# Optimization experiments

Measured on AMD Instinct MI355X. Metric: run time of the kernel, lower is better.

## Reference

```python
import jax, jax.numpy as jnp
import numpy as np

H, I = 16, 64
SCALE = 1.0 / (I ** 0.5)

def _rel_shift(x):
    # x: (S, J, B, H) -> Transformer-XL relative shift trick
    S, J, B, Hh = x.shape
    pad = jnp.zeros((S, 1, B, Hh), dtype=x.dtype)
    y = jnp.concatenate([pad, x], axis=1)           # (S, J+1, B, H)
    y = y.reshape(J + 1, S, B, Hh)[1:]              # (J, S, B, H)
    return y.reshape(S, J, B, Hh)

def setup_inputs() -> dict:
    key = jax.random.key(0)
    ks = jax.random.split(key, 10)
    S, P, B, E = 1024, 1024, 4, 1024
    J = P + S
    # causal mask: query s may attend keys j <= P + s; True = blocked
    mask = (jnp.arange(J)[None, :] > (P + jnp.arange(S))[:, None])[..., None]  # (S,J,1) bool
    sc = E ** -0.5
    return {
        "inputMHA": jax.random.normal(ks[0], (S, B, E), jnp.float32),
        "posEmbeddings": jax.random.normal(ks[1], (J, E), jnp.float32),
        "memory": jax.random.normal(ks[2], (P, B, E), jnp.float32),
        "u": jax.random.normal(ks[3], (H, I), jnp.float32) * 0.02,
        "v": jax.random.normal(ks[4], (H, I), jnp.float32) * 0.02,
        "mask": mask,
        "W_kv": jax.random.normal(ks[5], (E, 2 * H * I), jnp.float32) * sc,
        "W_q": jax.random.normal(ks[6], (E, H * I), jnp.float32) * sc,
        "W_p": jax.random.normal(ks[7], (E, H * I), jnp.float32) * sc,
        "W_o": jax.random.normal(ks[8], (H * I, E), jnp.float32) * sc,
        "gamma": jnp.ones((E,), jnp.float32),
        "beta": jnp.zeros((E,), jnp.float32),
    }

def reference(inputMHA, posEmbeddings, memory, u, v, mask, W_kv, W_q, W_p, W_o, gamma, beta):
    S, B, E = inputMHA.shape
    P = memory.shape[0]
    J = P + S
    x = jnp.concatenate([memory, inputMHA], axis=0)          # (J,B,E)
    kv = x @ W_kv                                            # (J,B,2HI)
    keys, values = jnp.split(kv, 2, axis=-1)
    q = (inputMHA @ W_q).reshape(S, B, H, I)                 # (S,B,H,I)
    K = keys.reshape(J, B, H, I)
    content = jnp.einsum('sbhi,jbhi->sjbh', q + u, K)        # content score
    p = (posEmbeddings @ W_p).reshape(J, H, I)               # (J,H,I)
    pos = jnp.einsum('sbhi,jhi->sjbh', q + v, p)             # position score
    pos = _rel_shift(pos)
    attn = content + pos                                     # (S,J,B,H)
    attn = jnp.where(mask[..., None], -jnp.inf, attn)        # mask (S,J,1)->(S,J,1,1)
    attn = jax.nn.softmax(attn * jnp.asarray(SCALE, attn.dtype), axis=1)
    V = values.reshape(J, B, H, I)
    awv = jnp.einsum('sjbh,jbhi->sbhi', attn, V).reshape(S, B, H * I)
    out = inputMHA + awv @ W_o                               # residual (dropout = eval identity)
    mean = jnp.mean(out, axis=-1, keepdims=True)
    var = jnp.var(out, axis=-1, keepdims=True)
    return (out - mean) / jnp.sqrt(var + 1e-5) * gamma + beta
```

## Files before the change

### kernel.cpp

```cpp
#include <hip/hip_runtime.h>
#include <hip/hip_bf16.h>

#define S_ 1024
#define P_ 1024
#define B_ 4
#define E_ 1024
#define J_ 2048
#define H_ 16
#define I_ 64

typedef __bf16 bf16_t;
typedef __bf16 bf16x8 __attribute__((ext_vector_type(8)));
typedef __bf16 bf16x4 __attribute__((ext_vector_type(4)));
typedef unsigned short u16x8 __attribute__((ext_vector_type(8)));
typedef float f32x4 __attribute__((ext_vector_type(4)));

#define MFMA16(a, b, c) __builtin_amdgcn_mfma_f32_16x16x32_bf16(a, b, c, 0, 0, 0)

#define SWZ(r, c) (((r) << 6) + ((((((c) >> 3)) ^ ((r) & 7)) << 3)) + ((c) & 7))

__device__ __forceinline__ void g2l16(const bf16_t* g, bf16_t* l) {
    __builtin_amdgcn_global_load_lds(
        (const __attribute__((address_space(1))) unsigned int*)(const void*)g,
        (__attribute__((address_space(3))) unsigned int*)(void*)l,
        16, 0, 0);
}

__global__ __launch_bounds__(256) void cvt_all_kernel(const float* __restrict__ memory,
                                                      const float* __restrict__ input,
                                                      const float* __restrict__ posEmb,
                                                      bf16_t* __restrict__ Xbf,
                                                      bf16_t* __restrict__ Pemb) {
    int blk = blockIdx.x;
    const float* src;
    bf16_t* dst;
    if (blk < 4096) { src = memory; dst = Xbf; }
    else if (blk < 8192) { blk -= 4096; src = input; dst = Xbf + (size_t)P_ * B_ * E_; }
    else { blk -= 8192; src = posEmb; dst = Pemb; }
    int i = (blk * 256 + threadIdx.x) * 4;
    float4 v = *(const float4*)(src + i);
    bf16x4 o = {(bf16_t)v.x, (bf16_t)v.y, (bf16_t)v.z, (bf16_t)v.w};
    *(bf16x4*)(dst + i) = o;
}

__global__ void trans_all_kernel(const float* __restrict__ W_kv, bf16_t* __restrict__ Wkvt,
                                 const float* __restrict__ W_q, bf16_t* __restrict__ Wqt,
                                 const float* __restrict__ W_p, bf16_t* __restrict__ Wpt,
                                 const float* __restrict__ W_o, bf16_t* __restrict__ Wot) {
    __shared__ float tile[32][33];
    int z = blockIdx.z;
    const float* W = (z == 0) ? W_kv : (z == 1) ? W_q : (z == 2) ? W_p : W_o;
    bf16_t* Wt = (z == 0) ? Wkvt : (z == 1) ? Wqt : (z == 2) ? Wpt : Wot;
    int N = (z == 0) ? 2048 : 1024;
    if (blockIdx.x * 32 >= N) return;
    int n0 = blockIdx.x * 32, k0 = blockIdx.y * 32;
    int x = threadIdx.x, y = threadIdx.y;
    for (int i = 0; i < 32; i += 8)
        tile[y + i][x] = W[(size_t)(k0 + y + i) * N + n0 + x];
    __syncthreads();
    for (int i = 0; i < 32; i += 8)
        Wt[(size_t)(n0 + y + i) * 1024 + k0 + x] = (bf16_t)tile[x][y + i];
}

__device__ __forceinline__ void gemm_tile(
    const bf16_t* __restrict__ A, const bf16_t* __restrict__ Bt, int N,
    int m0, int n0, int epi,
    bf16_t* __restrict__ out0, bf16_t* __restrict__ out1,
    const float* __restrict__ add0, const float* __restrict__ add1,
    float* __restrict__ outf,
    bf16_t* AlL, bf16_t* BlL) {
    const int K = 1024;
    int tid = threadIdx.x;
    int wave = tid >> 6, lane = tid & 63, quad = lane >> 4, l16 = lane & 15;
    int wm = (wave & 1) * 64, wn = (wave >> 1) * 64;
    int lrow = lane >> 3;
    int gsw = ((lane & 7) ^ lrow) << 3;
    f32x4 zero = {0.f, 0.f, 0.f, 0.f};
    f32x4 acc[4][4];
    #pragma unroll
    for (int i = 0; i < 4; i++)
        #pragma unroll
        for (int j = 0; j < 4; j++) acc[i][j] = zero;

    for (int k0 = 0; k0 < K; k0 += 64) {
        __syncthreads();
        #pragma unroll
        for (int r = 0; r < 4; r++) {
            int row0 = r * 32 + wave * 8;
            g2l16(&A[(size_t)(m0 + row0 + lrow) * K + k0 + gsw], &AlL[row0 * 64]);
            g2l16(&Bt[(size_t)(n0 + row0 + lrow) * K + k0 + gsw], &BlL[row0 * 64]);
        }
        __syncthreads();
        #pragma unroll
        for (int ks = 0; ks < 2; ks++) {
            bf16x8 af[4], bfr[4];
            #pragma unroll
            for (int i = 0; i < 4; i++)
                af[i] = *(const bf16x8*)&AlL[SWZ(wm + i * 16 + l16, ks * 32 + quad * 8)];
            #pragma unroll
            for (int j = 0; j < 4; j++)
                bfr[j] = *(const bf16x8*)&BlL[SWZ(wn + j * 16 + l16, ks * 32 + quad * 8)];
            #pragma unroll
            for (int i = 0; i < 4; i++)
                #pragma unroll
                for (int j = 0; j < 4; j++) acc[i][j] = MFMA16(af[i], bfr[j], acc[i][j]);
        }
    }
    #pragma unroll
    for (int i = 0; i < 4; i++)
        #pragma unroll
        for (int j = 0; j < 4; j++)
            #pragma unroll
            for (int reg = 0; reg < 4; reg++) {
                int m = m0 + wm + i * 16 + quad * 4 + reg;
                int n = n0 + wn + j * 16 + l16;
                float v = acc[i][j][reg];
                if (epi == 0) {
                    out0[(size_t)m * N + n] = (bf16_t)v;
                } else if (epi == 1) {
                    out0[(size_t)m * N + n] = (bf16_t)(v + add0[n]);
                    out1[(size_t)m * N + n] = (bf16_t)(v + add1[n]);
                } else {
                    outf[(size_t)m * N + n] = v + add0[(size_t)m * N + n];
                }
            }
}

__global__ __launch_bounds__(256) void gemm3_kernel(
    const bf16_t* __restrict__ Xbf, const bf16_t* __restrict__ Wkvt, bf16_t* __restrict__ kvb,
    const bf16_t* __restrict__ Wqt, bf16_t* __restrict__ qub, bf16_t* __restrict__ qvb,
    const float* __restrict__ u, const float* __restrict__ v,
    const bf16_t* __restrict__ Pemb, const bf16_t* __restrict__ Wpt, bf16_t* __restrict__ pb) {
    __shared__ __attribute__((aligned(16))) bf16_t Al[128 * 64];
    __shared__ __attribute__((aligned(16))) bf16_t Bl[128 * 64];
    int id = blockIdx.x;
    if (id < 1024) {
        gemm_tile(Xbf, Wkvt, 2048, (id >> 4) * 128, (id & 15) * 128, 0,
                  kvb, nullptr, nullptr, nullptr, nullptr, Al, Bl);
    } else if (id < 1280) {
        int t = id - 1024;
        gemm_tile(Xbf + (size_t)P_ * B_ * E_, Wqt, 1024, (t >> 3) * 128, (t & 7) * 128, 1,
                  qub, qvb, u, v, nullptr, Al, Bl);
    } else {
        int t = id - 1280;
        gemm_tile(Pemb, Wpt, 1024, (t >> 3) * 128, (t & 7) * 128, 0,
                  pb, nullptr, nullptr, nullptr, nullptr, Al, Bl);
    }
}

__global__ __launch_bounds__(256) void gemmo_kernel(
    const bf16_t* __restrict__ awvb, const bf16_t* __restrict__ Wot,
    const float* __restrict__ inputMHA, float* __restrict__ opre) {
    __shared__ __attribute__((aligned(16))) bf16_t Al[128 * 64];
    __shared__ __attribute__((aligned(16))) bf16_t Bl[128 * 64];
    int id = blockIdx.x;
    gemm_tile(awvb, Wot, 1024, (id >> 3) * 128, (id & 7) * 128, 2,
              nullptr, nullptr, inputMHA, nullptr, opre, Al, Bl);
}

__global__ __launch_bounds__(256) void flash_kernel(
    const bf16_t* __restrict__ qu, const bf16_t* __restrict__ qv,
    const bf16_t* __restrict__ kv, const bf16_t* __restrict__ pm,
    float* __restrict__ Oacc, float* __restrict__ lacc) {
    __shared__ __attribute__((aligned(16))) bf16_t Klds[64 * 64];
    __shared__ __attribute__((aligned(16))) bf16_t Vt[64 * 64];
    __shared__ __attribute__((aligned(16))) bf16_t Plds[128 * 64];
    __shared__ __attribute__((aligned(16))) bf16_t Prob[4 * 16 * 64];

    int tid = threadIdx.x;
    int wave = tid >> 6, lane = tid & 63, quad = lane >> 4, l16 = lane & 15;

    int x = blockIdx.x;
    int s_blk, c;
    if (x < 24) { s_blk = x / 3; c = x - s_blk * 3; }
    else        { int y = x - 24; s_blk = 8 + (y >> 2); c = y & 3; }
    int nt = 17 + s_blk;
    int t0 = c * 8;
    int t1 = t0 + 8; if (t1 > nt) t1 = nt;

    int s0 = s_blk * 64;
    int bh = blockIdx.y;
    int b = bh >> 4, h = bh & 15;
    int srow0 = s0 + wave * 16;

    const bf16_t* qub = qu + ((size_t)(srow0 + l16) * B_ + b) * 1024 + h * 64 + quad * 8;
    const bf16_t* qvb = qv + ((size_t)(srow0 + l16) * B_ + b) * 1024 + h * 64 + quad * 8;
    bf16x8 aqu0 = *(const bf16x8*)(qub);
    bf16x8 aqu1 = *(const bf16x8*)(qub + 32);
    bf16x8 aqv0 = *(const bf16x8*)(qvb);
    bf16x8 aqv1 = *(const bf16x8*)(qvb + 32);

    f32x4 zero = {0.f, 0.f, 0.f, 0.f};
    f32x4 accO[4];
    #pragma unroll
    for (int ot = 0; ot < 4; ot++) accO[ot] = zero;
    float lrowp[4] = {0.f, 0.f, 0.f, 0.f};

    const int w0u = 960 - s0;
    const int woff = 48 - wave * 16;
    const float SCL = 0.125f * 1.44269504088896f;

    int jr = tid >> 3, seg8g = tid & 7;
    int jp = tid & 31, iseg = tid >> 5;
    uint* VtU = (uint*)&Vt[0];
    bf16_t* ProbW = Prob + (wave << 10);

    {
        int j0 = t0 * 64;
        const bf16_t* kp = kv + ((size_t)(j0 + jr) * B_ + b) * 2048 + h * 64 + seg8g * 8;
        uint4 ka = *(const uint4*)kp;
        uint4 kb = *(const uint4*)(kp + (size_t)32 * B_ * 2048);
        const bf16_t* vp = kv + ((size_t)(j0 + jp * 2) * B_ + b) * 2048 + 1024 + h * 64 + iseg * 8;
        u16x8 va = *(const u16x8*)vp;
        u16x8 vb = *(const u16x8*)(vp + (size_t)B_ * 2048);
        uint4 pd[4];
        #pragma unroll
        for (int r = 0; r < 4; r++) {
            int idx = tid + 256 * r;
            int pr = idx >> 3, pg = idx & 7;
            int lr = w0u + j0 + pr; if (lr > J_ - 1) lr = J_ - 1;
            pd[r] = *(const uint4*)(pm + (size_t)lr * 1024 + h * 64 + pg * 8);
        }
        *(uint4*)&Klds[SWZ(jr, seg8g * 8)] = ka;
        *(uint4*)&Klds[SWZ(jr + 32, seg8g * 8)] = kb;
        #pragma unroll
        for (int e = 0; e < 8; e++) {
            int row = iseg * 8 + e;
            VtU[(row << 5) + ((((jp >> 2) ^ (row & 7)) << 2)) + (jp & 3)] =
                (uint)va[e] | ((uint)vb[e] << 16);
        }
        #pragma unroll
        for (int r = 0; r < 4; r++) {
            int idx = tid + 256 * r;
            int pr = idx >> 3, pg = idx & 7;
            *(uint4*)&Plds[SWZ((w0u + j0 + pr) & 127, pg * 8)] = pd[r];
        }
    }
    __syncthreads();

    for (int it = t0; it < t1; it++) {
        int j0 = it * 64;
        bool pf = (it + 1 < t1);
        uint4 ka, kb, pd0, pd1;
        u16x8 va, vb;
        int pr0 = tid >> 3, pg0 = tid & 7;
        int pr1 = (tid + 256) >> 3, pg1 = tid & 7;
        if (pf) {
            int j1 = j0 + 64;
            const bf16_t* kp = kv + ((size_t)(j1 + jr) * B_ + b) * 2048 + h * 64 + seg8g * 8;
            ka = *(const uint4*)kp;
            kb = *(const uint4*)(kp + (size_t)32 * B_ * 2048);
            const bf16_t* vp = kv + ((size_t)(j1 + jp * 2) * B_ + b) * 2048 + 1024 + h * 64 + iseg * 8;
            va = *(const u16x8*)vp;
            vb = *(const u16x8*)(vp + (size_t)B_ * 2048);
            int lr0 = w0u + j0 + 128 + pr0; if (lr0 > J_ - 1) lr0 = J_ - 1;
            int lr1 = w0u + j0 + 128 + pr1; if (lr1 > J_ - 1) lr1 = J_ - 1;
            pd0 = *(const uint4*)(pm + (size_t)lr0 * 1024 + h * 64 + pg0 * 8);
            pd1 = *(const uint4*)(pm + (size_t)lr1 * 1024 + h * 64 + pg1 * 8);
        }

        f32x4 cs[4];
        #pragma unroll
        for (int t = 0; t < 4; t++) cs[t] = zero;
        __builtin_amdgcn_s_setprio(1);
        #pragma unroll
        for (int ks = 0; ks < 2; ks++) {
            bf16x8 aq = ks ? aqu1 : aqu0;
            #pragma unroll
            for (int t = 0; t < 4; t++) {
                bf16x8 bk = *(const bf16x8*)&Klds[SWZ(t * 16 + l16, ks * 32 + quad * 8)];
                cs[t] = MFMA16(aq, bk, cs[t]);
            }
        }
        f32x4 ep[5];
        #pragma unroll
        for (int t = 0; t < 5; t++) ep[t] = zero;
        #pragma unroll
        for (int ks = 0; ks < 2; ks++) {
            bf16x8 aq = ks ? aqv1 : aqv0;
            #pragma unroll
            for (int t = 0; t < 5; t++) {
                int prow = (w0u + j0 + woff + t * 16 + l16) & 127;
                bf16x8 bp = *(const bf16x8*)&Plds[SWZ(prow, ks * 32 + quad * 8)];
                ep[t] = MFMA16(aq, bp, ep[t]);
            }
        }
        __builtin_amdgcn_s_setprio(0);

        #pragma unroll
        for (int reg = 0; reg < 4; reg++) {
            int r = quad * 4 + reg;
            int s = srow0 + r;
            int idx = l16 + 15 - r;
            int srcl = quad * 16 + (idx & 15);
            float sh[5];
            #pragma unroll
            for (int t = 0; t < 5; t++) sh[t] = __shfl(ep[t][reg], srcl);
            float psum = 0.f;
            #pragma unroll
            for (int t = 0; t < 4; t++) {
                float pos = (idx < 16) ? sh[t] : sh[t + 1];
                float p = exp2f((cs[t][reg] + pos) * SCL);
                p = (j0 + t * 16 + l16 > P_ + s) ? 0.f : p;
                ProbW[SWZ(r, t * 16 + l16)] = (bf16_t)p;
                psum += p;
            }
            lrowp[reg] += psum;
        }

        __builtin_amdgcn_s_setprio(1);
        #pragma unroll
        for (int ks = 0; ks < 2; ks++) {
            bf16x8 pa = *(const bf16x8*)&Prob[(wave << 10) + SWZ(l16, ks * 32 + quad * 8)];
            #pragma unroll
            for (int ot = 0; ot < 4; ot++) {
                bf16x8 bv = *(const bf16x8*)&Vt[SWZ(ot * 16 + l16, ks * 32 + quad * 8)];
                accO[ot] = MFMA16(pa, bv, accO[ot]);
            }
        }
        __builtin_amdgcn_s_setprio(0);

        __syncthreads();
        if (pf) {
            *(uint4*)&Klds[SWZ(jr, seg8g * 8)] = ka;
            *(uint4*)&Klds[SWZ(jr + 32, seg8g * 8)] = kb;
            #pragma unroll
            for (int e2 = 0; e2 < 8; e2++) {
                int row = iseg * 8 + e2;
                VtU[(row << 5) + ((((jp >> 2) ^ (row & 7)) << 2)) + (jp & 3)] =
                    (uint)va[e2] | ((uint)vb[e2] << 16);
            }
            *(uint4*)&Plds[SWZ((w0u + j0 + pr0) & 127, pg0 * 8)] = pd0;
            *(uint4*)&Plds[SWZ((w0u + j0 + pr1) & 127, pg1 * 8)] = pd1;
        }
        __syncthreads();
    }

    #pragma unroll
    for (int reg = 0; reg < 4; reg++) {
        int r = quad * 4 + reg;
        int srow = srow0 + r;
        float l = lrowp[reg];
        #pragma unroll
        for (int d = 1; d < 16; d <<= 1) l += __shfl_xor(l, d);
        if (l16 == 0) atomicAdd(&lacc[((size_t)srow * B_ + b) * H_ + h], l);
        size_t rowoff = ((size_t)srow * B_ + b) * 1024 + h * 64;
        #pragma unroll
        for (int ot = 0; ot < 4; ot++)
            atomicAdd(&Oacc[rowoff + ot * 16 + l16], accO[ot][reg]);
    }
}

__global__ __launch_bounds__(256) void norm_kernel(const float* __restrict__ Oacc,
                                                   const float* __restrict__ lacc,
                                                   bf16_t* __restrict__ awv) {
    int i4 = (blockIdx.x * 256 + threadIdx.x) * 4;
    int row = i4 >> 6;
    float inv = 1.0f / lacc[row];
    float4 o = *(const float4*)(Oacc + i4);
    bf16x4 r = {(bf16_t)(o.x * inv), (bf16_t)(o.y * inv),
                (bf16_t)(o.z * inv), (bf16_t)(o.w * inv)};
    *(bf16x4*)(awv + i4) = r;
}

__global__ __launch_bounds__(256) void ln_kernel(const float* __restrict__ x,
                                                 const float* __restrict__ gamma,
                                                 const float* __restrict__ beta,
                                                 float* __restrict__ out) {
    int row = blockIdx.x, tid = threadIdx.x;
    int lane = tid & 63, wave = tid >> 6;
    float4 v = ((const float4*)(x + (size_t)row * 1024))[tid];
    float s = v.x + v.y + v.z + v.w;
    float ss = v.x * v.x + v.y * v.y + v.z * v.z + v.w * v.w;
    #pragma unroll
    for (int sh = 1; sh < 64; sh <<= 1) { s += __shfl_xor(s, sh); ss += __shfl_xor(ss, sh); }
    __shared__ float red[8];
    if (lane == 0) { red[wave] = s; red[4 + wave] = ss; }
    __syncthreads();
    s = red[0] + red[1] + red[2] + red[3];
    ss = red[4] + red[5] + red[6] + red[7];
    float mean = s * (1.f / 1024.f);
    float var = ss * (1.f / 1024.f) - mean * mean;
    float inv = rsqrtf(var + 1e-5f);
    float4 g = ((const float4*)gamma)[tid];
    float4 bt = ((const float4*)beta)[tid];
    float4 o;
    o.x = (v.x - mean) * inv * g.x + bt.x;
    o.y = (v.y - mean) * inv * g.y + bt.y;
    o.z = (v.z - mean) * inv * g.z + bt.z;
    o.w = (v.w - mean) * inv * g.w + bt.w;
    ((float4*)(out + (size_t)row * 1024))[tid] = o;
}

extern "C" void kernel_launch(void* const* d_in, const int* in_sizes, int n_in,
                              void* d_out, int out_size, void* d_ws, size_t ws_size,
                              hipStream_t stream) {
    const float* inputMHA = (const float*)d_in[0];
    const float* posEmb   = (const float*)d_in[1];
    const float* memory   = (const float*)d_in[2];
    const float* u        = (const float*)d_in[3];
    const float* v        = (const float*)d_in[4];
    const float* W_kv     = (const float*)d_in[6];
    const float* W_q      = (const float*)d_in[7];
    const float* W_p      = (const float*)d_in[8];
    const float* W_o      = (const float*)d_in[9];
    const float* gamma    = (const float*)d_in[10];
    const float* beta     = (const float*)d_in[11];
    float* out = (float*)d_out;

    char* ws = (char*)d_ws;
    size_t off = 0;
    auto alloc = [&](size_t bytes) -> void* {
        void* p = ws + off;
        off += (bytes + 255) & ~(size_t)255;
        return p;
    };
    bf16_t* Xbf  = (bf16_t*)alloc((size_t)J_ * B_ * E_ * 2);
    bf16_t* Wkvt = (bf16_t*)alloc((size_t)2048 * 1024 * 2);
    bf16_t* Wqt  = (bf16_t*)alloc((size_t)1024 * 1024 * 2);
    bf16_t* Wpt  = (bf16_t*)alloc((size_t)1024 * 1024 * 2);
    bf16_t* Wot  = (bf16_t*)alloc((size_t)1024 * 1024 * 2);
    bf16_t* Pemb = (bf16_t*)alloc((size_t)2048 * 1024 * 2);
    bf16_t* kvb  = (bf16_t*)alloc((size_t)8192 * 2048 * 2);
    bf16_t* qub  = (bf16_t*)alloc((size_t)4096 * 1024 * 2);
    bf16_t* qvb  = (bf16_t*)alloc((size_t)4096 * 1024 * 2);
    bf16_t* pb   = (bf16_t*)alloc((size_t)2048 * 1024 * 2);
    bf16_t* awvb = (bf16_t*)alloc((size_t)4096 * 1024 * 2);
    float*  opre = (float*)alloc((size_t)4096 * 1024 * 4);
    float*  Oacc = (float*)alloc((size_t)4096 * 1024 * 4);
    float*  lacc = (float*)alloc((size_t)S_ * B_ * H_ * 4);

    hipMemsetAsync(Oacc, 0, (size_t)4096 * 1024 * 4, stream);
    hipMemsetAsync(lacc, 0, (size_t)S_ * B_ * H_ * 4, stream);

    cvt_all_kernel<<<10240, 256, 0, stream>>>(memory, inputMHA, posEmb, Xbf, Pemb);
    trans_all_kernel<<<dim3(64, 32, 4), dim3(32, 8), 0, stream>>>(
        W_kv, Wkvt, W_q, Wqt, W_p, Wpt, W_o, Wot);

    gemm3_kernel<<<1408, 256, 0, stream>>>(Xbf, Wkvt, kvb, Wqt, qub, qvb, u, v, Pemb, Wpt, pb);

    flash_kernel<<<dim3(56, B_ * H_), 256, 0, stream>>>(qub, qvb, kvb, pb, Oacc, lacc);
    norm_kernel<<<4096, 256, 0, stream>>>(Oacc, lacc, awvb);

    gemmo_kernel<<<256, 256, 0, stream>>>(awvb, Wot, inputMHA, opre);
    ln_kernel<<<S_ * B_, 256, 0, stream>>>(opre, gamma, beta, out);
}
```

Measured before the change: 433.0 us.

## Drop split-KV atomics in flash attention, fuse normalization, add XCD-aware block mapping

Each flash block now processes the full key range for its query tile instead of splitting it into chunks merged with float atomics. This lets the kernel normalize by the row sum and write bf16 output directly, which removes the Oacc/lacc buffers, their memsets and the separate norm kernel. Blocks are remapped on a 1D grid of 1024 so each XCD handles a group of batch-heads, and query tiles are paired long with short to balance causal work. The trade-off is fewer, longer blocks (1024 instead of 3584), so latency hiding and load balance now depend entirely on the pairing.

```diff
diff --git a/kernel.cpp b/kernel.cpp
--- a/kernel.cpp
+++ b/kernel.cpp
@@ -161,7 +161,7 @@
 __global__ __launch_bounds__(256) void flash_kernel(
     const bf16_t* __restrict__ qu, const bf16_t* __restrict__ qv,
     const bf16_t* __restrict__ kv, const bf16_t* __restrict__ pm,
-    float* __restrict__ Oacc, float* __restrict__ lacc) {
+    bf16_t* __restrict__ awv) {
     __shared__ __attribute__((aligned(16))) bf16_t Klds[64 * 64];
     __shared__ __attribute__((aligned(16))) bf16_t Vt[64 * 64];
     __shared__ __attribute__((aligned(16))) bf16_t Plds[128 * 64];
@@ -170,16 +170,17 @@
     int tid = threadIdx.x;
     int wave = tid >> 6, lane = tid & 63, quad = lane >> 4, l16 = lane & 15;
 
-    int x = blockIdx.x;
-    int s_blk, c;
-    if (x < 24) { s_blk = x / 3; c = x - s_blk * 3; }
-    else        { int y = x - 24; s_blk = 8 + (y >> 2); c = y & 3; }
+    int linear = blockIdx.x;
+    int xcd = linear & 7;
+    int p = linear >> 3;
+    int bh = xcd * 8 + ((p >> 2) & 7);
+    int q4 = ((p >> 5) << 2) | (p & 3);
+    int s_blk = (q4 < 8) ? q4 : 23 - q4;
     int nt = 17 + s_blk;
-    int t0 = c * 8;
-    int t1 = t0 + 8; if (t1 > nt) t1 = nt;
+    int t0 = 0;
+    int t1 = nt;
 
     int s0 = s_blk * 64;
-    int bh = blockIdx.y;
     int b = bh >> 4, h = bh & 15;
     int srow0 = s0 + wave * 16;
 
@@ -300,10 +301,10 @@
             #pragma unroll
             for (int t = 0; t < 4; t++) {
                 float pos = (idx < 16) ? sh[t] : sh[t + 1];
-                float p = exp2f((cs[t][reg] + pos) * SCL);
-                p = (j0 + t * 16 + l16 > P_ + s) ? 0.f : p;
-                ProbW[SWZ(r, t * 16 + l16)] = (bf16_t)p;
-                psum += p;
+                float p2 = exp2f((cs[t][reg] + pos) * SCL);
+                p2 = (j0 + t * 16 + l16 > P_ + s) ? 0.f : p2;
+                ProbW[SWZ(r, t * 16 + l16)] = (bf16_t)p2;
+                psum += p2;
             }
             lrowp[reg] += psum;
         }
@@ -343,24 +344,12 @@
         float l = lrowp[reg];
         #pragma unroll
         for (int d = 1; d < 16; d <<= 1) l += __shfl_xor(l, d);
-        if (l16 == 0) atomicAdd(&lacc[((size_t)srow * B_ + b) * H_ + h], l);
+        float inv = 1.0f / l;
         size_t rowoff = ((size_t)srow * B_ + b) * 1024 + h * 64;
         #pragma unroll
         for (int ot = 0; ot < 4; ot++)
-            atomicAdd(&Oacc[rowoff + ot * 16 + l16], accO[ot][reg]);
+            awv[rowoff + ot * 16 + l16] = (bf16_t)(accO[ot][reg] * inv);
     }
-}
-
-__global__ __launch_bounds__(256) void norm_kernel(const float* __restrict__ Oacc,
-                                                   const float* __restrict__ lacc,
-                                                   bf16_t* __restrict__ awv) {
-    int i4 = (blockIdx.x * 256 + threadIdx.x) * 4;
-    int row = i4 >> 6;
-    float inv = 1.0f / lacc[row];
-    float4 o = *(const float4*)(Oacc + i4);
-    bf16x4 r = {(bf16_t)(o.x * inv), (bf16_t)(o.y * inv),
-                (bf16_t)(o.z * inv), (bf16_t)(o.w * inv)};
-    *(bf16x4*)(awv + i4) = r;
 }
 
 __global__ __launch_bounds__(256) void ln_kernel(const float* __restrict__ x,
@@ -427,11 +416,6 @@
     bf16_t* pb   = (bf16_t*)alloc((size_t)2048 * 1024 * 2);
     bf16_t* awvb = (bf16_t*)alloc((size_t)4096 * 1024 * 2);
     float*  opre = (float*)alloc((size_t)4096 * 1024 * 4);
-    float*  Oacc = (float*)alloc((size_t)4096 * 1024 * 4);
-    float*  lacc = (float*)alloc((size_t)S_ * B_ * H_ * 4);
-
-    hipMemsetAsync(Oacc, 0, (size_t)4096 * 1024 * 4, stream);
-    hipMemsetAsync(lacc, 0, (size_t)S_ * B_ * H_ * 4, stream);
 
     cvt_all_kernel<<<10240, 256, 0, stream>>>(memory, inputMHA, posEmb, Xbf, Pemb);
     trans_all_kernel<<<dim3(64, 32, 4), dim3(32, 8), 0, stream>>>(
@@ -439,8 +423,7 @@
 
     gemm3_kernel<<<1408, 256, 0, stream>>>(Xbf, Wkvt, kvb, Wqt, qub, qvb, u, v, Pemb, Wpt, pb);
 
-    flash_kernel<<<dim3(56, B_ * H_), 256, 0, stream>>>(qub, qvb, kvb, pb, Oacc, lacc);
-    norm_kernel<<<4096, 256, 0, stream>>>(Oacc, lacc, awvb);
+    flash_kernel<<<1024, 256, 0, stream>>>(qub, qvb, kvb, pb, awvb);
 
     gemmo_kernel<<<256, 256, 0, stream>>>(awvb, Wot, inputMHA, opre);
     ln_kernel<<<S_ * B_, 256, 0, stream>>>(opre, gamma, beta, out);
```

Result: faster. 383.4 us (-11.5%).
